# Kernel optimization log

Measured on AMD Instinct MI355X. Metric: run time of the kernel, lower is better.

Reference implementation:

```python
import jax, jax.numpy as jnp
import numpy as np

DIM = 384
HEADS = 12
WS = (2, 7, 7)
SS = (1, 3, 3)
B, D, H, W = 4, 8, 56, 56
N = WS[0] * WS[1] * WS[2]  # 98


def _win_part_np(x, ws):
    b, d, h, w, c = x.shape
    x = x.reshape(b, d // ws[0], ws[0], h // ws[1], ws[1], w // ws[2], ws[2], c)
    return x.transpose(0, 1, 3, 5, 2, 4, 6, 7).reshape(-1, ws[0] * ws[1] * ws[2], c)


def setup_inputs() -> dict:
    key = jax.random.key(0)
    ks = jax.random.split(key, 6)
    s = 0.02
    x = jax.random.normal(ks[0], (B, D, H, W, DIM), jnp.float32)
    # relative position index (static int buffer)
    coords = np.stack(np.meshgrid(np.arange(WS[0]), np.arange(WS[1]), np.arange(WS[2]), indexing='ij')).reshape(3, -1)
    rel = (coords[:, :, None] - coords[:, None, :]).transpose(1, 2, 0)
    rel[..., 0] += WS[0] - 1
    rel[..., 1] += WS[1] - 1
    rel[..., 2] += WS[2] - 1
    rel[..., 0] *= (2 * WS[1] - 1) * (2 * WS[2] - 1)
    rel[..., 1] *= 2 * WS[2] - 1
    rel_index = jnp.asarray(rel.sum(-1), jnp.int32)  # [N, N]
    # shifted-window attention mask (standard Swin construction)
    img = np.zeros((1, D, H, W, 1), np.float32)
    cnt = 0
    for dsl in (slice(0, -WS[0]), slice(-WS[0], -SS[0]), slice(-SS[0], None)):
        for hsl in (slice(0, -WS[1]), slice(-WS[1], -SS[1]), slice(-SS[1], None)):
            for wsl in (slice(0, -WS[2]), slice(-WS[2], -SS[2]), slice(-SS[2], None)):
                img[:, dsl, hsl, wsl, :] = cnt
                cnt += 1
    mw = _win_part_np(img, WS).squeeze(-1)  # [nW, N]
    attn_mask = np.where(mw[:, None, :] != mw[:, :, None], -100.0, 0.0).astype(np.float32)
    table_size = (2 * WS[0] - 1) * (2 * WS[1] - 1) * (2 * WS[2] - 1)
    return {
        'x': x,
        'mask': jnp.asarray(attn_mask),
        'rel_table': jax.random.normal(ks[1], (table_size, HEADS), jnp.float32) * s,
        'rel_index': rel_index,
        'qkv_w': jax.random.normal(ks[2], (3 * DIM, DIM), jnp.float32) * s,
        'qkv_b': jnp.zeros((3 * DIM,), jnp.float32),
        'proj_w': jax.random.normal(ks[3], (DIM, DIM), jnp.float32) * s,
        'proj_b': jnp.zeros((DIM,), jnp.float32),
        'g1': jnp.ones((DIM,), jnp.float32), 'b1': jnp.zeros((DIM,), jnp.float32),
        'g2': jnp.ones((DIM,), jnp.float32), 'b2': jnp.zeros((DIM,), jnp.float32),
        'fc1_w': jax.random.normal(ks[4], (DIM, DIM), jnp.float32) * s,
        'fc1_b': jnp.zeros((DIM,), jnp.float32),
        'fc2_w': jax.random.normal(ks[5], (DIM, DIM), jnp.float32) * s,
        'fc2_b': jnp.zeros((DIM,), jnp.float32),
    }


def _ln(x, g, b, eps=1e-5):
    mu = x.mean(-1, keepdims=True)
    var = jnp.mean((x - mu) ** 2, axis=-1, keepdims=True)
    return (x - mu) * jax.lax.rsqrt(var + eps) * g + b


def _window_partition(x, ws):
    b, d, h, w, c = x.shape
    x = x.reshape(b, d // ws[0], ws[0], h // ws[1], ws[1], w // ws[2], ws[2], c)
    return x.transpose(0, 1, 3, 5, 2, 4, 6, 7).reshape(-1, ws[0] * ws[1] * ws[2], c)


def _window_reverse(win, ws, b, d, h, w):
    x = win.reshape(b, d // ws[0], h // ws[1], w // ws[2], ws[0], ws[1], ws[2], -1)
    return x.transpose(0, 1, 4, 2, 5, 3, 6, 7).reshape(b, d, h, w, -1)


def reference(x, mask, rel_table, rel_index, qkv_w, qkv_b, proj_w, proj_b,
              g1, b1, g2, b2, fc1_w, fc1_b, fc2_w, fc2_b):
    shortcut = x
    h = _ln(x, g1, b1)
    b, d, hh, ww, c = h.shape
    # get_window_size: clamp window/shift to input extents (static here)
    ws = [min(WS[i], (d, hh, ww)[i]) for i in range(3)]
    ss = [0 if (d, hh, ww)[i] <= WS[i] else SS[i] for i in range(3)]
    pad = [(ws[i] - (d, hh, ww)[i] % ws[i]) % ws[i] for i in range(3)]
    h = jnp.pad(h, ((0, 0), (0, pad[0]), (0, pad[1]), (0, pad[2]), (0, 0)))
    dp, hp, wp = h.shape[1:4]
    if any(ss):
        h = jnp.roll(h, shift=(-ss[0], -ss[1], -ss[2]), axis=(1, 2, 3))
    xw = _window_partition(h, ws)  # [B_, N, C]
    bw, n, _ = xw.shape
    hd = c // HEADS
    qkv = (xw @ qkv_w.T + qkv_b).reshape(bw, n, 3, HEADS, hd).transpose(2, 0, 3, 1, 4)
    q, k, v = qkv[0], qkv[1], qkv[2]  # [B_, H, N, hd]
    scale = hd ** -0.5
    attn = jnp.einsum('bhnd,bhmd->bhnm', q * scale, k)
    bias = rel_table[rel_index[:n, :n].reshape(-1)].reshape(n, n, HEADS).transpose(2, 0, 1)
    attn = attn + bias[None]
    nW = mask.shape[0]
    attn = attn.reshape(bw // nW, nW, HEADS, n, n) + mask[None, :, None]
    attn = jax.nn.softmax(attn.reshape(bw, HEADS, n, n), axis=-1)
    out = jnp.einsum('bhnm,bhmd->bhnd', attn, v).transpose(0, 2, 1, 3).reshape(bw, n, c)
    out = out @ proj_w.T + proj_b
    out = _window_reverse(out, ws, b, dp, hp, wp)
    if any(ss):
        out = jnp.roll(out, shift=(ss[0], ss[1], ss[2]), axis=(1, 2, 3))
    out = out[:, :d, :hh, :ww, :]
    x1 = shortcut + out
    h2 = _ln(x1, g2, b2)
    mlp = jax.nn.gelu(h2 @ fc1_w.T + fc1_b, approximate=False) @ fc2_w.T + fc2_b
    return x1 + mlp
```

## Files before the change

kernel.cpp:

```cpp
#include <hip/hip_runtime.h>
#include <hip/hip_bf16.h>

#define HEADS 12
#define NWIN 1024
#define NW_MASK 256
#define NTOK 98
#define CDIM 384
#define NROWS (NWIN * NTOK)
#define QKVN (3 * CDIM)
#define PSTR 136
#define LOG2E 1.4426950408889634f
#define SCALE_LOG2E 0.25503486f

using u16 = unsigned short;
typedef __attribute__((ext_vector_type(8))) short short8;
typedef __attribute__((ext_vector_type(4))) short s16x4;
typedef __attribute__((ext_vector_type(4))) float f32x4;
typedef __attribute__((ext_vector_type(2))) unsigned u32x2;

__device__ __forceinline__ float b2f(u16 u) { return __uint_as_float(((unsigned)u) << 16); }
__device__ __forceinline__ u16 f2b(float f) {
  unsigned u = __float_as_uint(f);
  u += 0x7FFF + ((u >> 16) & 1);
  return (u16)(u >> 16);
}

__device__ __forceinline__ int tok_of_row(int r) {
  int win = r / NTOK;
  int j   = r - win * NTOK;
  int b   = win >> 8;
  int wl  = win & 255;
  int wd = wl >> 6, wh = (wl >> 3) & 7, ww = wl & 7;
  int od = j / 49; int rem = j - od * 49;
  int oh = rem / 7; int ow = rem - oh * 7;
  int sd = (wd * 2 + od + 1) & 7;
  int sh = wh * 7 + oh + 3; if (sh >= 56) sh -= 56;
  int sw = ww * 7 + ow + 3; if (sw >= 56) sw -= 56;
  return ((b * 8 + sd) * 56 + sh) * 56 + sw;
}

__device__ __forceinline__ int xcd_swz(int bid, int nwg) {
  int q = nwg >> 3, r = nwg & 7;
  int xcd = bid & 7, i = bid >> 3;
  return ((xcd < r) ? xcd * (q + 1) : r * (q + 1) + (xcd - r) * q) + i;
}

__global__ void detect_kernel(const unsigned* __restrict__ g1w, int* __restrict__ flag) {
  if (threadIdx.x == 0 && blockIdx.x == 0)
    flag[0] = (g1w[0] == 0x3F800000u) ? 1 : 0;
}

__device__ __forceinline__ float raw_at(const void* src, size_t j, int isf32) {
  return isf32 ? ((const float*)src)[j] : b2f(((const u16*)src)[j]);
}

struct CvtArgs {
  const void* src[12];
  unsigned off[13];
};
__global__ __launch_bounds__(256) void cvt_all(CvtArgs a, u16* __restrict__ dst,
                                               const int* __restrict__ flag) {
  int i = blockIdx.x * 256 + threadIdx.x;
  if (i >= (int)a.off[12]) return;
  int s = 0;
#pragma unroll
  for (int k = 1; k < 12; ++k) s += (i >= (int)a.off[k]);
  int j = i - (int)a.off[s];
  dst[i] = flag[0] ? f2b(((const float*)a.src[s])[j]) : ((const u16*)a.src[s])[j];
}

__global__ __launch_bounds__(256) void ln_kernel(const void* __restrict__ in,
                                                 const u16* __restrict__ gam,
                                                 const u16* __restrict__ bet,
                                                 u16* __restrict__ outp,
                                                 u16* __restrict__ xg,
                                                 const int* __restrict__ flag) {
  int wrow = blockIdx.x * 4 + (threadIdx.x >> 6);
  int lane = threadIdx.x & 63;
  int isf32 = flag[0];
  size_t srow = (size_t)tok_of_row(wrow);
  const u16*   ip16 = (const u16*)in + srow * CDIM;
  const float* ip32 = (const float*)in + srow * CDIM;
  float xv[6]; float s = 0.f, s2 = 0.f;
#pragma unroll
  for (int i = 0; i < 6; ++i) {
    int c = lane + 64 * i;
    xv[i] = isf32 ? ip32[c] : b2f(ip16[c]);
    s += xv[i]; s2 += xv[i] * xv[i];
  }
#pragma unroll
  for (int off = 1; off < 64; off <<= 1) {
    s  += __shfl_xor(s, off);
    s2 += __shfl_xor(s2, off);
  }
  float mu = s * (1.f / CDIM);
  float var = s2 * (1.f / CDIM) - mu * mu;
  float rstd = rsqrtf(var + 1e-5f);
  u16* op = outp + (size_t)wrow * CDIM;
  u16* xp = xg + (size_t)wrow * CDIM;
#pragma unroll
  for (int i = 0; i < 6; ++i) {
    int c = lane + 64 * i;
    xp[c] = f2b(xv[i]);
    op[c] = f2b((xv[i] - mu) * rstd * b2f(gam[c]) + b2f(bet[c]));
  }
}

__global__ void prep_kernel(const void* __restrict__ msrc, u16* __restrict__ mdst,
                            const void* __restrict__ tab, const int* __restrict__ idx,
                            float* __restrict__ biasf, const int* __restrict__ flag,
                            float* __restrict__ st2) {
  int i = blockIdx.x * 256 + threadIdx.x;
  int isf32 = flag[0];
  if (i < 2 * NROWS) st2[i] = 0.f;
  if (i < HEADS * NTOK * 100) {
    int h = i / (NTOK * 100);
    int rem = i - h * (NTOK * 100);
    int q = rem / 100, t = rem - q * 100;
    biasf[i] = (t < NTOK) ? raw_at(tab, (size_t)idx[q * NTOK + t] * HEADS + h, isf32) * LOG2E : 0.f;
  }
  if (i >= NW_MASK * NTOK * 100) return;
  int w = i / (NTOK * 100);
  int rem = i - w * (NTOK * 100);
  int q = rem / 100, t = rem - q * 100;
  mdst[i] = (t < NTOK) ? f2b(raw_at(msrc, (size_t)(w * NTOK + q) * NTOK + t, isf32) * LOG2E)
                       : (u16)0;
}

__device__ __forceinline__ void gload16(const u16* g, u16* l) {
  __builtin_amdgcn_global_load_lds((const __attribute__((address_space(1))) unsigned*)g,
                                   (__attribute__((address_space(3))) unsigned*)l,
                                   16, 0, 0);
}

template<int EPI, bool SWZ>
__global__ __launch_bounds__(256) void gemm_bt(const u16* __restrict__ A, int lda,
                                               const u16* __restrict__ W,
                                               const u16* __restrict__ bias,
                                               int NB, void* __restrict__ outb, int ldo,
                                               const void* __restrict__ aux,
                                               const int* __restrict__ flag,
                                               float* __restrict__ stats,
                                               const u16* __restrict__ lng,
                                               const u16* __restrict__ lnb) {
  __shared__ __align__(16) u16 lA[128 * 32];
  __shared__ __align__(16) u16 lB[128 * 32];
  int bid = SWZ ? xcd_swz(blockIdx.x, gridDim.x) : blockIdx.x;
  int mb = bid / NB, nb = bid - mb * NB;
  int row0 = mb * 128, col0 = nb * 128;
  int tid = threadIdx.x;
  int lane = tid & 63;
  int wid = tid >> 6;
  int wr = (wid >> 1) * 64, wc = (wid & 1) * 64;
  f32x4 zero = {0.f, 0.f, 0.f, 0.f};
  f32x4 acc[4][4];
#pragma unroll
  for (int m = 0; m < 4; ++m)
#pragma unroll
    for (int n = 0; n < 4; ++n) acc[m][n] = zero;

  int e0 = tid * 8;
  int e1 = 2048 + tid * 8;
  int r0 = e0 >> 5, c0 = e0 & 31;
  int r1 = e1 >> 5, c1 = e1 & 31;
  int g = (lane >> 4) * 8, fr = lane & 15;

  float mu_[4], rs_[4];
  if (EPI == 2) {
#pragma unroll
    for (int m = 0; m < 4; ++m) {
      int rr = row0 + wr + m * 16 + fr;
      float sv = stats[2 * rr], qv = stats[2 * rr + 1];
      float mu = sv * (1.f / CDIM);
      float var = qv * (1.f / CDIM) - mu * mu;
      mu_[m] = mu;
      rs_[m] = rsqrtf(var + 1e-5f);
    }
  }

  for (int kt = 0; kt < CDIM; kt += 32) {
    gload16(&A[(size_t)(row0 + r0) * lda + kt + c0], &lA[e0]);
    gload16(&A[(size_t)(row0 + r1) * lda + kt + c1], &lA[e1]);
    gload16(&W[(size_t)(col0 + r0) * CDIM + kt + c0], &lB[e0]);
    gload16(&W[(size_t)(col0 + r1) * CDIM + kt + c1], &lB[e1]);
    __syncthreads();
    short8 af[4], bf[4];
#pragma unroll
    for (int m = 0; m < 4; ++m) af[m] = *(const short8*)&lA[(wr + m * 16 + fr) * 32 + g];
#pragma unroll
    for (int n = 0; n < 4; ++n) bf[n] = *(const short8*)&lB[(wc + n * 16 + fr) * 32 + g];
    if (EPI == 2) {
      short8 gv = *(const short8*)&lng[kt + g];
      short8 bv8 = *(const short8*)&lnb[kt + g];
#pragma unroll
      for (int m = 0; m < 4; ++m) {
        short8 a = af[m], o;
#pragma unroll
        for (int i = 0; i < 8; ++i) {
          float f = (b2f((u16)a[i]) - mu_[m]) * rs_[m] * b2f((u16)gv[i]) + b2f((u16)bv8[i]);
          o[i] = (short)f2b(f);
        }
        af[m] = o;
      }
    }
#pragma unroll
    for (int m = 0; m < 4; ++m)
#pragma unroll
      for (int n = 0; n < 4; ++n)
        acc[m][n] = __builtin_amdgcn_mfma_f32_16x16x32_bf16(af[m], bf[n], acc[m][n], 0, 0, 0);
    __syncthreads();
  }

  int isf32 = (EPI == 3) ? flag[0] : 0;
  int colo = lane & 15;
  int rowo = (lane >> 4) * 4;
  float bv[4];
#pragma unroll
  for (int n = 0; n < 4; ++n) bv[n] = b2f(bias[col0 + wc + n * 16 + colo]);
#pragma unroll
  for (int m = 0; m < 4; ++m) {
#pragma unroll
    for (int r = 0; r < 4; ++r) {
      int gr = row0 + wr + m * 16 + rowo + r;
      int t = (EPI == 3) ? tok_of_row(gr) : 0;
      float ps = 0.f, ps2 = 0.f;
#pragma unroll
      for (int n = 0; n < 4; ++n) {
        int gc = col0 + wc + n * 16 + colo;
        float v = acc[m][n][r] + bv[n];
        if (EPI == 0) {
          ((u16*)outb)[(size_t)gr * ldo + gc] = f2b(v);
        } else if (EPI == 1) {
          float xs = b2f(((const u16*)aux)[(size_t)gr * CDIM + gc]);
          float o = v + xs;
          ((u16*)outb)[(size_t)gr * ldo + gc] = f2b(o);
          ps += o; ps2 += o * o;
        } else if (EPI == 2) {
          float ge = 0.5f * v * (1.f + erff(v * 0.70710678118654752f));
          ((u16*)outb)[(size_t)gr * ldo + gc] = f2b(ge);
        } else {
          float x1v = b2f(((const u16*)aux)[(size_t)gr * CDIM + gc]);
          float o = v + x1v;
          if (isf32) ((float*)outb)[(size_t)t * CDIM + gc] = o;
          else       ((u16*)outb)[(size_t)t * CDIM + gc] = f2b(o);
        }
      }
      if (EPI == 1) {
#pragma unroll
        for (int off = 1; off < 16; off <<= 1) {
          ps  += __shfl_xor(ps, off);
          ps2 += __shfl_xor(ps2, off);
        }
        if (colo == 0) {
          atomicAdd(&stats[2 * gr],     ps);
          atomicAdd(&stats[2 * gr + 1], ps2);
        }
      }
    }
  }
}

__global__ __launch_bounds__(256, 3) void attn_mfma(u16* __restrict__ qkv,
                                                    const u16* __restrict__ maskp,
                                                    const float* __restrict__ biasf) {
  __shared__ __align__(16) u16 P4[4][16 * PSTR];
  int wid = threadIdx.x >> 6, lane = threadIdx.x & 63;
  int gh = blockIdx.x * 4 + wid;
  int win = gh / HEADS, hd = gh - win * HEADS;
  int l15 = lane & 15, g = lane >> 4;
  u16* P = P4[wid];
  const size_t base = (size_t)win * NTOK * QKVN + (size_t)hd * 32;
  u16* qp = qkv + base;
  const u16* kp = qkv + base + CDIM;
  const u16* vp = qkv + base + 2 * CDIM;
  const f32x4 zero = {0.f, 0.f, 0.f, 0.f};

  { u32x2 z = {0u, 0u}; *(u32x2*)&P[l15 * PSTR + 112 + 4 * g] = z; }

  short8 kf[7];
#pragma unroll
  for (int n = 0; n < 7; ++n) {
    int tok = n * 16 + l15; if (tok > NTOK - 1) tok = NTOK - 1;
    kf[n] = *(const short8*)&kp[(size_t)tok * QKVN + 8 * g];
  }
  short8 vf[2][4];
#pragma unroll
  for (int kk = 0; kk < 4; ++kk)
#pragma unroll
    for (int i = 0; i < 8; ++i) {
      int tok = 32 * kk + 8 * g + i;
      const u16* vr = vp + (size_t)tok * QKVN + l15;
      u16 v0 = (tok < NTOK) ? vr[0]  : (u16)0;
      u16 v1 = (tok < NTOK) ? vr[16] : (u16)0;
      vf[0][kk][i] = (short)v0;
      vf[1][kk][i] = (short)v1;
    }

  const float* brow = biasf + (size_t)hd * NTOK * 100;
  const u16*   mrow = maskp + (size_t)(win & (NW_MASK - 1)) * NTOK * 100;

  for (int m = 0; m < 7; ++m) {
    int qrow = m * 16 + l15;
    int qr = qrow > NTOK - 1 ? NTOK - 1 : qrow;
    short8 qf = *(const short8*)&qp[(size_t)qr * QKVN + 8 * g];
    f32x4 st[7];
#pragma unroll
    for (int n = 0; n < 7; ++n)
      st[n] = __builtin_amdgcn_mfma_f32_16x16x32_bf16(kf[n], qf, zero, 0, 0, 0);

    float pv[7][4];
    float sum = 0.f;
#pragma unroll
    for (int n = 0; n < 7; ++n) {
      f32x4 bb = *(const f32x4*)&brow[(size_t)qr * 100 + n * 16 + 4 * g];
      s16x4 mm = *(const s16x4*)&mrow[(size_t)qr * 100 + n * 16 + 4 * g];
#pragma unroll
      for (int r = 0; r < 4; ++r) {
        int tok = n * 16 + 4 * g + r;
        float s = st[n][r] * SCALE_LOG2E + bb[r] + b2f((u16)mm[r]);
        if (tok > NTOK - 1) s = -1e30f;
        float e = exp2f(s);
        pv[n][r] = e; sum += e;
      }
    }
    sum += __shfl_xor(sum, 16);
    sum += __shfl_xor(sum, 32);
    float inv = 1.f / sum;
#pragma unroll
    for (int n = 0; n < 7; ++n) {
      __hip_bfloat162 h0 = __float22bfloat162_rn(make_float2(pv[n][0] * inv, pv[n][1] * inv));
      __hip_bfloat162 h1 = __float22bfloat162_rn(make_float2(pv[n][2] * inv, pv[n][3] * inv));
      u32x2 wv = { *(unsigned*)&h0, *(unsigned*)&h1 };
      *(u32x2*)&P[l15 * PSTR + n * 16 + 4 * g] = wv;
    }
    f32x4 oa0 = zero, oa1 = zero;
#pragma unroll
    for (int kk = 0; kk < 4; ++kk) {
      short8 pf = *(const short8*)&P[l15 * PSTR + kk * 32 + 8 * g];
      oa0 = __builtin_amdgcn_mfma_f32_16x16x32_bf16(pf, vf[0][kk], oa0, 0, 0, 0);
      oa1 = __builtin_amdgcn_mfma_f32_16x16x32_bf16(pf, vf[1][kk], oa1, 0, 0, 0);
    }
#pragma unroll
    for (int r = 0; r < 4; ++r) {
      int row = m * 16 + 4 * g + r;
      if (row < NTOK) {
        qp[(size_t)row * QKVN + l15]      = f2b(oa0[r]);
        qp[(size_t)row * QKVN + 16 + l15] = f2b(oa1[r]);
      }
    }
  }
}

extern "C" void kernel_launch(void* const* d_in, const int* in_sizes, int n_in,
                              void* d_out, int out_size, void* d_ws, size_t ws_size,
                              hipStream_t stream) {
  (void)n_in; (void)out_size; (void)ws_size;
  const void* x    = d_in[0];
  const int* ridx  = (const int*)d_in[3];

  char* ws = (char*)d_ws;
  const size_t SZ_QKV = (size_t)NROWS * QKVN * 2;
  const size_t SZ_MAT = (size_t)NROWS * CDIM * 2;
  const size_t SZ_BIAS = (size_t)HEADS * NTOK * 100 * 4;
  const size_t SZ_MASKP = (size_t)NW_MASK * NTOK * 100 * 2;
  u16* qkv     = (u16*)ws;
  u16* bufA    = (u16*)(ws + SZ_QKV);
  u16* bufX1   = (u16*)(ws + SZ_QKV + SZ_MAT);
  float* biasf = (float*)(ws + SZ_QKV + 2 * SZ_MAT);
  u16* maskp   = (u16*)(ws + SZ_QKV + 2 * SZ_MAT + SZ_BIAS);
  int* flag    = (int*)(ws + SZ_QKV + 2 * SZ_MAT + SZ_BIAS + SZ_MASKP);
  u16* cvt     = (u16*)((char*)flag + 256);
  float* stats2 = (float*)((char*)flag + 256 + 2 * 1024 * 1024);

  detect_kernel<<<1, 64, 0, stream>>>((const unsigned*)d_in[8], flag);

  CvtArgs ca;
  unsigned off = 0;
  u16* cp[16];
  for (int k = 0; k < 12; ++k) {
    int i = 4 + k;
    ca.src[k] = d_in[i];
    ca.off[k] = off;
    cp[i] = cvt + off;
    off += (unsigned)in_sizes[i];
  }
  ca.off[12] = off;
  cvt_all<<<(off + 255) / 256, 256, 0, stream>>>(ca, cvt, flag);

  prep_kernel<<<(NW_MASK * NTOK * 100 + 255) / 256, 256, 0, stream>>>(
      d_in[1], maskp, d_in[2], ridx, biasf, flag, stats2);
  ln_kernel<<<NROWS / 4, 256, 0, stream>>>(x, cp[8], cp[9], bufA, bufX1, flag);
  gemm_bt<0, true><<<(NROWS / 128) * (QKVN / 128), 256, 0, stream>>>(
      bufA, CDIM, cp[4], cp[5], QKVN / 128, qkv, QKVN, nullptr, flag, nullptr, nullptr, nullptr);
  attn_mfma<<<(NWIN * HEADS) / 4, 256, 0, stream>>>(qkv, maskp, biasf);
  gemm_bt<1, true><<<(NROWS / 128) * (CDIM / 128), 256, 0, stream>>>(
      qkv, QKVN, cp[6], cp[7], CDIM / 128, bufX1, CDIM, bufX1, flag, stats2, nullptr, nullptr);
  gemm_bt<2, true><<<(NROWS / 128) * (CDIM / 128), 256, 0, stream>>>(
      bufX1, CDIM, cp[12], cp[13], CDIM / 128, bufA, CDIM, nullptr, flag, stats2, cp[10], cp[11]);
  gemm_bt<3, true><<<(NROWS / 128) * (CDIM / 128), 256, 0, stream>>>(
      bufA, CDIM, cp[14], cp[15], CDIM / 128, d_out, CDIM, bufX1, flag, nullptr, nullptr, nullptr);
}
```

Baseline: 688.0 us.

## Fuse QKV projection into per-window attention kernel

Replaces the separate QKV GEMM and attention kernel with one kernel per window that loads the LayerNorm output tile into LDS, computes K, V and Q per head with MFMA, and runs softmax attention directly. This removes the write and re-read of the large qkv intermediate in global memory. In exchange, weights are re-read per window from cache, LDS use limits occupancy to one block per CU, and register pressure rises.

After: 781.6 us. +13.6%, slower.

```diff
diff --git a/kernel.cpp b/kernel.cpp
--- a/kernel.cpp
+++ b/kernel.cpp
@@ -9,6 +9,8 @@
 #define NROWS (NWIN * NTOK)
 #define QKVN (3 * CDIM)
 #define PSTR 136
+#define ASTR 392
+#define KSTR 36
 #define LOG2E 1.4426950408889634f
 #define SCALE_LOG2E 0.25503486f
 
@@ -228,9 +230,7 @@
       for (int n = 0; n < 4; ++n) {
         int gc = col0 + wc + n * 16 + colo;
         float v = acc[m][n][r] + bv[n];
-        if (EPI == 0) {
-          ((u16*)outb)[(size_t)gr * ldo + gc] = f2b(v);
-        } else if (EPI == 1) {
+        if (EPI == 1) {
           float xs = b2f(((const u16*)aux)[(size_t)gr * CDIM + gc]);
           float o = v + xs;
           ((u16*)outb)[(size_t)gr * ldo + gc] = f2b(o);
@@ -260,92 +260,168 @@
   }
 }
 
-__global__ __launch_bounds__(256, 3) void attn_mfma(u16* __restrict__ qkv,
-                                                    const u16* __restrict__ maskp,
-                                                    const float* __restrict__ biasf) {
-  __shared__ __align__(16) u16 P4[4][16 * PSTR];
-  int wid = threadIdx.x >> 6, lane = threadIdx.x & 63;
-  int gh = blockIdx.x * 4 + wid;
-  int win = gh / HEADS, hd = gh - win * HEADS;
+__global__ __launch_bounds__(256, 1) void qkv_attn(const u16* __restrict__ A,
+                                                   const u16* __restrict__ wqkv,
+                                                   const u16* __restrict__ bqkv,
+                                                   u16* __restrict__ O,
+                                                   const u16* __restrict__ maskp,
+                                                   const float* __restrict__ biasf) {
+  __shared__ __align__(16) u16 Al[98 * ASTR];
+  __shared__ __align__(16) u16 Kl[4][98 * KSTR];
+  __shared__ __align__(16) u16 Vl[4][98 * KSTR];
+  __shared__ __align__(16) u16 Ql[4][16 * KSTR];
+  __shared__ __align__(16) u16 Pl[4][16 * PSTR];
+  int tid = threadIdx.x, lane = tid & 63, wid = tid >> 6;
+  int win = blockIdx.x;
   int l15 = lane & 15, g = lane >> 4;
-  u16* P = P4[wid];
-  const size_t base = (size_t)win * NTOK * QKVN + (size_t)hd * 32;
-  u16* qp = qkv + base;
-  const u16* kp = qkv + base + CDIM;
-  const u16* vp = qkv + base + 2 * CDIM;
   const f32x4 zero = {0.f, 0.f, 0.f, 0.f};
 
-  { u32x2 z = {0u, 0u}; *(u32x2*)&P[l15 * PSTR + 112 + 4 * g] = z; }
-
-  short8 kf[7];
-#pragma unroll
-  for (int n = 0; n < 7; ++n) {
-    int tok = n * 16 + l15; if (tok > NTOK - 1) tok = NTOK - 1;
-    kf[n] = *(const short8*)&kp[(size_t)tok * QKVN + 8 * g];
-  }
-  short8 vf[2][4];
-#pragma unroll
-  for (int kk = 0; kk < 4; ++kk)
-#pragma unroll
-    for (int i = 0; i < 8; ++i) {
-      int tok = 32 * kk + 8 * g + i;
-      const u16* vr = vp + (size_t)tok * QKVN + l15;
-      u16 v0 = (tok < NTOK) ? vr[0]  : (u16)0;
-      u16 v1 = (tok < NTOK) ? vr[16] : (u16)0;
-      vf[0][kk][i] = (short)v0;
-      vf[1][kk][i] = (short)v1;
-    }
-
-  const float* brow = biasf + (size_t)hd * NTOK * 100;
-  const u16*   mrow = maskp + (size_t)(win & (NW_MASK - 1)) * NTOK * 100;
-
-  for (int m = 0; m < 7; ++m) {
-    int qrow = m * 16 + l15;
-    int qr = qrow > NTOK - 1 ? NTOK - 1 : qrow;
-    short8 qf = *(const short8*)&qp[(size_t)qr * QKVN + 8 * g];
-    f32x4 st[7];
-#pragma unroll
-    for (int n = 0; n < 7; ++n)
-      st[n] = __builtin_amdgcn_mfma_f32_16x16x32_bf16(kf[n], qf, zero, 0, 0, 0);
-
-    float pv[7][4];
-    float sum = 0.f;
+  const u16* Ag = A + (size_t)win * NTOK * CDIM;
+  for (int c = tid; c < 98 * 48; c += 256) {
+    int row = c / 48, off = (c - row * 48) * 8;
+    *(short8*)&Al[row * ASTR + off] = *(const short8*)&Ag[row * 384 + off];
+  }
+  __syncthreads();
+
+  u16* Kw = Kl[wid];
+  u16* Vw = Vl[wid];
+  u16* Qw = Ql[wid];
+  u16* Pw = Pl[wid];
+
+  for (int hi = 0; hi < 3; ++hi) {
+    int hd = wid + hi * 4;
+#pragma unroll
+    for (int mat = 0; mat < 2; ++mat) {
+      const u16* wb = wqkv + (size_t)((mat ? 768 : 384) + hd * 32) * 384;
+      const u16* bb = bqkv + (mat ? 768 : 384) + hd * 32;
+      u16* dst = mat ? Vw : Kw;
+      short8 bf0[12], bf1[12];
+#pragma unroll
+      for (int kk = 0; kk < 12; ++kk) {
+        bf0[kk] = *(const short8*)&wb[(size_t)l15 * 384 + kk * 32 + 8 * g];
+        bf1[kk] = *(const short8*)&wb[(size_t)(16 + l15) * 384 + kk * 32 + 8 * g];
+      }
+      float b0 = b2f(bb[l15]), b1 = b2f(bb[16 + l15]);
+#pragma unroll
+      for (int m = 0; m < 7; ++m) {
+        int ar = m * 16 + l15; if (ar > NTOK - 1) ar = NTOK - 1;
+        short8 af[12];
+#pragma unroll
+        for (int kk = 0; kk < 12; ++kk) af[kk] = *(const short8*)&Al[ar * ASTR + kk * 32 + 8 * g];
+        f32x4 a0 = zero, a1 = zero;
+#pragma unroll
+        for (int kk = 0; kk < 12; ++kk) {
+          a0 = __builtin_amdgcn_mfma_f32_16x16x32_bf16(af[kk], bf0[kk], a0, 0, 0, 0);
+          a1 = __builtin_amdgcn_mfma_f32_16x16x32_bf16(af[kk], bf1[kk], a1, 0, 0, 0);
+        }
+#pragma unroll
+        for (int r = 0; r < 4; ++r) {
+          int row = m * 16 + 4 * g + r;
+          if (row < NTOK) {
+            dst[row * KSTR + l15]      = f2b(a0[r] + b0);
+            dst[row * KSTR + 16 + l15] = f2b(a1[r] + b1);
+          }
+        }
+      }
+    }
+
+    short8 kf[7];
 #pragma unroll
     for (int n = 0; n < 7; ++n) {
-      f32x4 bb = *(const f32x4*)&brow[(size_t)qr * 100 + n * 16 + 4 * g];
-      s16x4 mm = *(const s16x4*)&mrow[(size_t)qr * 100 + n * 16 + 4 * g];
+      int tok = n * 16 + l15; if (tok > NTOK - 1) tok = NTOK - 1;
+      kf[n] = *(const short8*)&Kw[tok * KSTR + 8 * g];
+    }
+    short8 vf[2][4];
+#pragma unroll
+    for (int kk = 0; kk < 4; ++kk)
+#pragma unroll
+      for (int i = 0; i < 8; ++i) {
+        int tok = 32 * kk + 8 * g + i;
+        u16 v0 = (tok < NTOK) ? Vw[tok * KSTR + l15]      : (u16)0;
+        u16 v1 = (tok < NTOK) ? Vw[tok * KSTR + 16 + l15] : (u16)0;
+        vf[0][kk][i] = (short)v0;
+        vf[1][kk][i] = (short)v1;
+      }
+    const u16* wq = wqkv + (size_t)(hd * 32) * 384;
+    short8 bq0[12], bq1[12];
+#pragma unroll
+    for (int kk = 0; kk < 12; ++kk) {
+      bq0[kk] = *(const short8*)&wq[(size_t)l15 * 384 + kk * 32 + 8 * g];
+      bq1[kk] = *(const short8*)&wq[(size_t)(16 + l15) * 384 + kk * 32 + 8 * g];
+    }
+    float qb0 = b2f(bqkv[hd * 32 + l15]), qb1 = b2f(bqkv[hd * 32 + 16 + l15]);
+
+    const float* brow = biasf + (size_t)hd * NTOK * 100;
+    const u16*   mrow = maskp + (size_t)(win & (NW_MASK - 1)) * NTOK * 100;
+    u16* Ow = O + (size_t)win * NTOK * CDIM + hd * 32;
+
+    { u32x2 z = {0u, 0u}; *(u32x2*)&Pw[l15 * PSTR + 112 + 4 * g] = z; }
+
+    for (int m = 0; m < 7; ++m) {
+      int ar = m * 16 + l15; if (ar > NTOK - 1) ar = NTOK - 1;
+      short8 af[12];
+#pragma unroll
+      for (int kk = 0; kk < 12; ++kk) af[kk] = *(const short8*)&Al[ar * ASTR + kk * 32 + 8 * g];
+      f32x4 q0 = zero, q1 = zero;
+#pragma unroll
+      for (int kk = 0; kk < 12; ++kk) {
+        q0 = __builtin_amdgcn_mfma_f32_16x16x32_bf16(af[kk], bq0[kk], q0, 0, 0, 0);
+        q1 = __builtin_amdgcn_mfma_f32_16x16x32_bf16(af[kk], bq1[kk], q1, 0, 0, 0);
+      }
 #pragma unroll
       for (int r = 0; r < 4; ++r) {
-        int tok = n * 16 + 4 * g + r;
-        float s = st[n][r] * SCALE_LOG2E + bb[r] + b2f((u16)mm[r]);
-        if (tok > NTOK - 1) s = -1e30f;
-        float e = exp2f(s);
-        pv[n][r] = e; sum += e;
-      }
-    }
-    sum += __shfl_xor(sum, 16);
-    sum += __shfl_xor(sum, 32);
-    float inv = 1.f / sum;
-#pragma unroll
-    for (int n = 0; n < 7; ++n) {
-      __hip_bfloat162 h0 = __float22bfloat162_rn(make_float2(pv[n][0] * inv, pv[n][1] * inv));
-      __hip_bfloat162 h1 = __float22bfloat162_rn(make_float2(pv[n][2] * inv, pv[n][3] * inv));
-      u32x2 wv = { *(unsigned*)&h0, *(unsigned*)&h1 };
-      *(u32x2*)&P[l15 * PSTR + n * 16 + 4 * g] = wv;
-    }
-    f32x4 oa0 = zero, oa1 = zero;
-#pragma unroll
-    for (int kk = 0; kk < 4; ++kk) {
-      short8 pf = *(const short8*)&P[l15 * PSTR + kk * 32 + 8 * g];
-      oa0 = __builtin_amdgcn_mfma_f32_16x16x32_bf16(pf, vf[0][kk], oa0, 0, 0, 0);
-      oa1 = __builtin_amdgcn_mfma_f32_16x16x32_bf16(pf, vf[1][kk], oa1, 0, 0, 0);
-    }
-#pragma unroll
-    for (int r = 0; r < 4; ++r) {
-      int row = m * 16 + 4 * g + r;
-      if (row < NTOK) {
-        qp[(size_t)row * QKVN + l15]      = f2b(oa0[r]);
-        qp[(size_t)row * QKVN + 16 + l15] = f2b(oa1[r]);
+        int rr = 4 * g + r;
+        Qw[rr * KSTR + l15]      = f2b(q0[r] + qb0);
+        Qw[rr * KSTR + 16 + l15] = f2b(q1[r] + qb1);
+      }
+      short8 qf = *(const short8*)&Qw[l15 * KSTR + 8 * g];
+
+      int qrow = m * 16 + l15;
+      int qr = qrow > NTOK - 1 ? NTOK - 1 : qrow;
+      f32x4 st[7];
+#pragma unroll
+      for (int n = 0; n < 7; ++n)
+        st[n] = __builtin_amdgcn_mfma_f32_16x16x32_bf16(kf[n], qf, zero, 0, 0, 0);
+
+      float pv[7][4];
+      float sum = 0.f;
+#pragma unroll
+      for (int n = 0; n < 7; ++n) {
+        f32x4 bb = *(const f32x4*)&brow[(size_t)qr * 100 + n * 16 + 4 * g];
+        s16x4 mm = *(const s16x4*)&mrow[(size_t)qr * 100 + n * 16 + 4 * g];
+#pragma unroll
+        for (int r = 0; r < 4; ++r) {
+          int tok = n * 16 + 4 * g + r;
+          float s = st[n][r] * SCALE_LOG2E + bb[r] + b2f((u16)mm[r]);
+          if (tok > NTOK - 1) s = -1e30f;
+          float e = exp2f(s);
+          pv[n][r] = e; sum += e;
+        }
+      }
+      sum += __shfl_xor(sum, 16);
+      sum += __shfl_xor(sum, 32);
+      float inv = 1.f / sum;
+#pragma unroll
+      for (int n = 0; n < 7; ++n) {
+        __hip_bfloat162 h0 = __float22bfloat162_rn(make_float2(pv[n][0] * inv, pv[n][1] * inv));
+        __hip_bfloat162 h1 = __float22bfloat162_rn(make_float2(pv[n][2] * inv, pv[n][3] * inv));
+        u32x2 wv = { *(unsigned*)&h0, *(unsigned*)&h1 };
+        *(u32x2*)&Pw[l15 * PSTR + n * 16 + 4 * g] = wv;
+      }
+      f32x4 oa0 = zero, oa1 = zero;
+#pragma unroll
+      for (int kk = 0; kk < 4; ++kk) {
+        short8 pf = *(const short8*)&Pw[l15 * PSTR + kk * 32 + 8 * g];
+        oa0 = __builtin_amdgcn_mfma_f32_16x16x32_bf16(pf, vf[0][kk], oa0, 0, 0, 0);
+        oa1 = __builtin_amdgcn_mfma_f32_16x16x32_bf16(pf, vf[1][kk], oa1, 0, 0, 0);
+      }
+#pragma unroll
+      for (int r = 0; r < 4; ++r) {
+        int row = m * 16 + 4 * g + r;
+        if (row < NTOK) {
+          Ow[(size_t)row * CDIM + l15]      = f2b(oa0[r]);
+          Ow[(size_t)row * CDIM + 16 + l15] = f2b(oa1[r]);
+        }
       }
     }
   }
@@ -363,7 +439,7 @@
   const size_t SZ_MAT = (size_t)NROWS * CDIM * 2;
   const size_t SZ_BIAS = (size_t)HEADS * NTOK * 100 * 4;
   const size_t SZ_MASKP = (size_t)NW_MASK * NTOK * 100 * 2;
-  u16* qkv     = (u16*)ws;
+  u16* bufO    = (u16*)ws;
   u16* bufA    = (u16*)(ws + SZ_QKV);
   u16* bufX1   = (u16*)(ws + SZ_QKV + SZ_MAT);
   float* biasf = (float*)(ws + SZ_QKV + 2 * SZ_MAT);
@@ -390,11 +466,9 @@
   prep_kernel<<<(NW_MASK * NTOK * 100 + 255) / 256, 256, 0, stream>>>(
       d_in[1], maskp, d_in[2], ridx, biasf, flag, stats2);
   ln_kernel<<<NROWS / 4, 256, 0, stream>>>(x, cp[8], cp[9], bufA, bufX1, flag);
-  gemm_bt<0, true><<<(NROWS / 128) * (QKVN / 128), 256, 0, stream>>>(
-      bufA, CDIM, cp[4], cp[5], QKVN / 128, qkv, QKVN, nullptr, flag, nullptr, nullptr, nullptr);
-  attn_mfma<<<(NWIN * HEADS) / 4, 256, 0, stream>>>(qkv, maskp, biasf);
+  qkv_attn<<<NWIN, 256, 0, stream>>>(bufA, cp[4], cp[5], bufO, maskp, biasf);
   gemm_bt<1, true><<<(NROWS / 128) * (CDIM / 128), 256, 0, stream>>>(
-      qkv, QKVN, cp[6], cp[7], CDIM / 128, bufX1, CDIM, bufX1, flag, stats2, nullptr, nullptr);
+      bufO, CDIM, cp[6], cp[7], CDIM / 128, bufX1, CDIM, bufX1, flag, stats2, nullptr, nullptr);
   gemm_bt<2, true><<<(NROWS / 128) * (CDIM / 128), 256, 0, stream>>>(
       bufX1, CDIM, cp[12], cp[13], CDIM / 128, bufA, CDIM, nullptr, flag, stats2, cp[10], cp[11]);
   gemm_bt<3, true><<<(NROWS / 128) * (CDIM / 128), 256, 0, stream>>>(
```
